# Performance work log

Hardware: AMD Instinct MI355X
Metric: run time of the kernel (lower is better)

The kernel has to match this reference:

```python
import jax, jax.numpy as jnp
import numpy as np

B, D, H, C = 8192, 1024, 4, 4  # batch, input_dim, num_heads, num_classes


def setup_inputs() -> dict:
    key = jax.random.key(0)
    ks = jax.random.split(key, 24)
    s = 0.02
    n = jax.random.normal
    d = {
        "X1": n(ks[0], (B, D), jnp.float32),
        "X2": n(ks[1], (B, D), jnp.float32),
        "X3": n(ks[2], (B, D), jnp.float32),
        "X4": n(ks[3], (B, D), jnp.float32),
        # shared Q projection (injected into both self- and cross-attn at init)
        "Wq": n(ks[4], (D, D), jnp.float32) * s,
        "bq": jnp.zeros((D,), jnp.float32),
        # self-attention K/V/out projections
        "Wk_s": n(ks[5], (D, D), jnp.float32) * s,
        "bk_s": jnp.zeros((D,), jnp.float32),
        "Wv_s": n(ks[6], (D, D), jnp.float32) * s,
        "bv_s": jnp.zeros((D,), jnp.float32),
        "Wo_s": n(ks[7], (D, D), jnp.float32) * s,
        "bo_s": jnp.zeros((D,), jnp.float32),
        # cross-attention K/V/out projections
        "Wk_c": n(ks[8], (D, D), jnp.float32) * s,
        "bk_c": jnp.zeros((D,), jnp.float32),
        "Wv_c": n(ks[9], (D, D), jnp.float32) * s,
        "bv_c": jnp.zeros((D,), jnp.float32),
        "Wo_c": n(ks[10], (D, D), jnp.float32) * s,
        "bo_c": jnp.zeros((D,), jnp.float32),
        # classifier
        "Wc": n(ks[11], (C, D), jnp.float32) * s,
        "bc": jnp.zeros((C,), jnp.float32),
    }
    return d


def _mha(q, kv, Wq, bq, Wk, bk, Wv, bv, Wo, bo):
    # q: (B, Lq, D), kv: (B, Lk, D); matches torch nn.MultiheadAttention math
    Bq, Lq, Dm = q.shape
    Lk = kv.shape[1]
    hd = Dm // H
    Q = (q @ Wq.T + bq).reshape(Bq, Lq, H, hd).transpose(0, 2, 1, 3)
    K = (kv @ Wk.T + bk).reshape(Bq, Lk, H, hd).transpose(0, 2, 1, 3)
    V = (kv @ Wv.T + bv).reshape(Bq, Lk, H, hd).transpose(0, 2, 1, 3)
    scores = jnp.einsum('bhqd,bhkd->bhqk', Q, K) / jnp.sqrt(jnp.float32(hd))
    attn = jax.nn.softmax(scores, axis=-1)
    out = jnp.einsum('bhqk,bhkd->bhqd', attn, V)
    out = out.transpose(0, 2, 1, 3).reshape(Bq, Lq, Dm)
    return out @ Wo.T + bo


def _diff_attn(query, key_list, p):
    # query: (B, D); key_list: list of 3 (B, D)
    q1 = query[:, None, :]  # (B, 1, D)
    self_out = _mha(q1, q1, p['Wq'], p['bq'], p['Wk_s'], p['bk_s'],
                    p['Wv_s'], p['bv_s'], p['Wo_s'], p['bo_s'])
    keys = jnp.stack(key_list, axis=1)          # (B, 3, D)
    differ_keys = q1 - keys                      # (B, 3, D)
    cross_out = _mha(q1, differ_keys, p['Wq'], p['bq'], p['Wk_c'], p['bk_c'],
                     p['Wv_c'], p['bv_c'], p['Wo_c'], p['bo_c'])
    return (self_out + cross_out)[:, 0]          # (B, D)


def reference(X1, X2, X3, X4, Wq, bq, Wk_s, bk_s, Wv_s, bv_s, Wo_s, bo_s,
              Wk_c, bk_c, Wv_c, bv_c, Wo_c, bo_c, Wc, bc):
    p = dict(Wq=Wq, bq=bq, Wk_s=Wk_s, bk_s=bk_s, Wv_s=Wv_s, bv_s=bv_s,
             Wo_s=Wo_s, bo_s=bo_s, Wk_c=Wk_c, bk_c=bk_c, Wv_c=Wv_c,
             bv_c=bv_c, Wo_c=Wo_c, bo_c=bo_c)
    d1 = _diff_attn(X1, [X2, X3, X4], p)
    d2 = _diff_attn(X2, [X1, X3, X4], p)
    d3 = _diff_attn(X3, [X1, X2, X4], p)
    d4 = _diff_attn(X4, [X1, X2, X3], p)
    features = jnp.concatenate([d1, d2, d3, d4], axis=0)  # (4B, D)
    logits = features @ Wc.T + bc                          # (4B, C)
    return (d1, d2, d3, d4, logits)
```

## Files before the change

### kernel.cpp

```cpp
#include <hip/hip_runtime.h>

typedef __bf16 bf16x8 __attribute__((ext_vector_type(8)));
typedef float f32x4 __attribute__((ext_vector_type(4)));

__device__ __forceinline__ float bf2f(unsigned short u) {
  union { unsigned int i; float f; } c; c.i = ((unsigned int)u) << 16; return c.f;
}
__device__ __forceinline__ unsigned short f2bf(float f) {
  union { float f; unsigned int i; } c; c.f = f;
  unsigned int u = c.i;
  u += 0x7FFFu + ((u >> 16) & 1u);
  return (unsigned short)(u >> 16);
}

#define GLDS16(g, l)                                                          \
  __builtin_amdgcn_global_load_lds(                                           \
      (const __attribute__((address_space(1))) void*)(g),                     \
      (__attribute__((address_space(3))) void*)(l), 16, 0, 0)

#define MFMA16(a, b, c) __builtin_amdgcn_mfma_f32_16x16x32_bf16(a, b, c, 0, 0, 0)


__global__ __launch_bounds__(256) void convert_x(
    const float* __restrict__ X1, const float* __restrict__ X2,
    const float* __restrict__ X3, const float* __restrict__ X4,
    unsigned short* __restrict__ Xcat)
{
  int gid = blockIdx.x * 256 + threadIdx.x;
  size_t base = (size_t)gid * 4;
  int sec = (int)(base >> 23);
  int off = (int)(base & 8388607);
  const float* s = sec == 0 ? X1 : sec == 1 ? X2 : sec == 2 ? X3 : X4;
  float4 v = *(const float4*)(s + off);
  ushort4 o;
  o.x = f2bf(v.x); o.y = f2bf(v.y); o.z = f2bf(v.z); o.w = f2bf(v.w);
  *(ushort4*)(Xcat + base) = o;
}

__global__ __launch_bounds__(256) void prep_w(
    const float* __restrict__ Wq,  const float* __restrict__ Wk_c,
    const float* __restrict__ Wv_c, const float* __restrict__ Wo_c,
    const float* __restrict__ Wo_s,
    unsigned short* __restrict__ Wcat, unsigned short* __restrict__ WoM2,
    unsigned short* __restrict__ Wos_bf)
{
  int gid = blockIdx.x * 256 + threadIdx.x;
  if (gid < 786432) {
    int base = gid * 4;
    int sec = base >> 20, off = base & 1048575;
    const float* s = sec == 0 ? Wk_c : sec == 1 ? Wv_c : Wq;
    float4 v = *(const float4*)(s + off);
    ushort4 o;
    o.x = f2bf(v.x); o.y = f2bf(v.y); o.z = f2bf(v.z); o.w = f2bf(v.w);
    *(ushort4*)(Wcat + base) = o;
  } else if (gid < 1048576) {
    int idx = (gid - 786432) * 4;
    int n = idx >> 10, c = idx & 1023;
    float4 v = *(const float4*)(Wo_c + (size_t)n * 1024 + c);
    ushort4 o;
    o.x = f2bf(v.x); o.y = f2bf(v.y); o.z = f2bf(v.z); o.w = f2bf(v.w);
    *(ushort4*)(WoM2 + (size_t)n * 2048 + c) = o;
  } else if (gid < 1310720) {
    int base = (gid - 1048576) * 4;
    float4 v = *(const float4*)(Wo_s + base);
    ushort4 o;
    o.x = f2bf(v.x); o.y = f2bf(v.y); o.z = f2bf(v.z); o.w = f2bf(v.w);
    *(ushort4*)(Wos_bf + base) = o;
  }
}

__global__ __launch_bounds__(256) void transpose_wvs(
    const float* __restrict__ Wv_s, unsigned short* __restrict__ WvsT)
{
  __shared__ float tile[32][33];
  const int r = threadIdx.x >> 3;
  const int c4 = (threadIdx.x & 7) * 4;
  const int j0 = blockIdx.y * 32, k0 = blockIdx.x * 32;
  float4 v = *(const float4*)(Wv_s + (size_t)(j0 + r) * 1024 + k0 + c4);
  tile[r][c4] = v.x; tile[r][c4 + 1] = v.y; tile[r][c4 + 2] = v.z; tile[r][c4 + 3] = v.w;
  __syncthreads();
  ushort4 o;
  o.x = f2bf(tile[c4 + 0][r]); o.y = f2bf(tile[c4 + 1][r]);
  o.z = f2bf(tile[c4 + 2][r]); o.w = f2bf(tile[c4 + 3][r]);
  *(ushort4*)(WvsT + (size_t)(k0 + r) * 1024 + j0 + c4) = o;
}

__global__ __launch_bounds__(256) void bias2_kernel(
    const float* __restrict__ Wo_s, const float* __restrict__ bv_s,
    const float* __restrict__ bo_c, const float* __restrict__ bo_s,
    float* __restrict__ bias2)
{
  const int wv = threadIdx.x >> 6, l = threadIdx.x & 63;
  const int n = blockIdx.x * 4 + wv;
  const float* row = Wo_s + (size_t)n * 1024;
  float s = 0.f;
#pragma unroll
  for (int it = 0; it < 4; ++it) {
    int j = it * 256 + l * 4;
    float4 w = *(const float4*)(row + j);
    float4 b = *(const float4*)(bv_s + j);
    s += w.x * b.x + w.y * b.y + w.z * b.z + w.w * b.w;
  }
#pragma unroll
  for (int d = 1; d < 64; d <<= 1) s += __shfl_xor(s, d);
  if (l == 0) bias2[n] = s + bo_c[n] + bo_s[n];
}

template<bool OUT_F32, bool HAS_BIAS>
__global__ __launch_bounds__(256) void gemm_bt(
    const unsigned short* __restrict__ A1, int lda1, int K1,
    const unsigned short* __restrict__ A2, int lda2, int K2,
    const unsigned short* __restrict__ Bw, int ldb,
    void* __restrict__ Cout, int ldc,
    const float* __restrict__ bias)
{
  __shared__ char lds[16384];
  char* ldsA = lds;
  char* ldsB = lds + 8192;

  const int t = threadIdx.x;
  const int l = t & 63;
  const int wv = t >> 6;
  const int wr = wv >> 1, wc = wv & 1;
  const int bM = blockIdx.y * 128, bN = blockIdx.x * 128;

  const int pa0 = t, pa1 = t + 256;
  const int ra0 = pa0 >> 2, ra1 = pa1 >> 2;
  const int ca0 = (((pa0 & 3) ^ ((ra0 >> 1) & 3))) * 8;
  const int ca1 = (((pa1 & 3) ^ ((ra1 >> 1) & 3))) * 8;
  const unsigned short* gB0 = Bw + (size_t)(bN + ra0) * ldb + ca0;
  const unsigned short* gB1 = Bw + (size_t)(bN + ra1) * ldb + ca1;
  char* lA0 = ldsA + pa0 * 16; char* lA1 = ldsA + pa1 * 16;
  char* lB0 = ldsB + pa0 * 16; char* lB1 = ldsB + pa1 * 16;

  const int rA = wr * 64 + (l & 15);
  const int rB = wc * 64 + (l & 15);
  const int cA = ((l >> 4) ^ ((rA >> 1) & 3)) * 16;
  const int cB = ((l >> 4) ^ ((rB >> 1) & 3)) * 16;
  const char* fA = ldsA + rA * 64 + cA;
  const char* fB = ldsB + rB * 64 + cB;

  f32x4 acc[4][4] = {};

  const unsigned short* gA0 = A1 + (size_t)(bM + ra0) * lda1 + ca0;
  const unsigned short* gA1 = A1 + (size_t)(bM + ra1) * lda1 + ca1;

  for (int src = 0; src < 2; ++src) {
    const int Kc = src ? K2 : K1;
    if (src) {
      if (K2 == 0) break;
      gA0 = A2 + (size_t)(bM + ra0) * lda2 + ca0;
      gA1 = A2 + (size_t)(bM + ra1) * lda2 + ca1;
    }
    for (int k0 = 0; k0 < Kc; k0 += 32) {
      GLDS16(gA0, lA0); GLDS16(gA1, lA1);
      GLDS16(gB0, lB0); GLDS16(gB1, lB1);
      gA0 += 32; gA1 += 32; gB0 += 32; gB1 += 32;
      __syncthreads();

      bf16x8 af[4], bfv[4];
#pragma unroll
      for (int i = 0; i < 4; ++i) af[i] = *(const bf16x8*)(fA + i * 1024);
#pragma unroll
      for (int i = 0; i < 4; ++i) bfv[i] = *(const bf16x8*)(fB + i * 1024);
#pragma unroll
      for (int mt = 0; mt < 4; ++mt)
#pragma unroll
        for (int nt = 0; nt < 4; ++nt)
          acc[mt][nt] = MFMA16(af[mt], bfv[nt], acc[mt][nt]);
      __syncthreads();
    }
  }

  const int mrow = bM + wr * 64 + ((l >> 4) << 2);
  const int ncol = bN + wc * 64 + (l & 15);
  float bvals[4];
  if (HAS_BIAS) {
#pragma unroll
    for (int nt = 0; nt < 4; ++nt) bvals[nt] = bias[ncol + nt * 16];
  }
#pragma unroll
  for (int mt = 0; mt < 4; ++mt)
#pragma unroll
    for (int nt = 0; nt < 4; ++nt)
#pragma unroll
      for (int r = 0; r < 4; ++r) {
        size_t idx = (size_t)(mrow + mt * 16 + r) * ldc + (ncol + nt * 16);
        float v = acc[mt][nt][r];
        if (HAS_BIAS) v += bvals[nt];
        if (OUT_F32) ((float*)Cout)[idx] = v;
        else         ((unsigned short*)Cout)[idx] = f2bf(v);
      }
}

template<bool OUT_F32, bool HAS_BIAS>
__global__ __launch_bounds__(512, 2) void gemm256(
    const unsigned short* __restrict__ A1, int lda1, int K1,
    const unsigned short* __restrict__ A2, int lda2, int K2,
    const unsigned short* __restrict__ Bw, int ldb,
    void* __restrict__ Cout, int ldc,
    const float* __restrict__ bias)
{
  __shared__ __align__(128) char lds[131072];

  const int tid = threadIdx.x;
  const int l  = tid & 63;
  const int wv = tid >> 6;
  const int wr = wv >> 2, wc = wv & 3;

  const int nN = gridDim.x;
  int lin = blockIdx.y * nN + blockIdx.x;
  int nwg = nN * gridDim.y;
  int id2 = ((nwg & 7) == 0) ? ((lin & 7) * (nwg >> 3) + (lin >> 3)) : lin;
  const int bM = (id2 / nN) * 256;
  const int bN = (id2 % nN) * 256;

  const int NT1 = K1 >> 6;
  const int NT  = (K1 + K2) >> 6;

  const int sr0  = tid >> 2;
  const int colE = ((tid & 3) ^ ((sr0 >> 1) & 3)) * 8;
  const unsigned short* pA1g0 = A1 + (size_t)(bM + sr0) * lda1 + colE;
  const unsigned short* pA1g1 = A1 + (size_t)(bM + sr0 + 128) * lda1 + colE;
  const unsigned short* pA2g0 = (K2 > 0) ? A2 + (size_t)(bM + sr0) * lda2 + colE : pA1g0;
  const unsigned short* pA2g1 = (K2 > 0) ? A2 + (size_t)(bM + sr0 + 128) * lda2 + colE : pA1g1;
  const unsigned short* pBg0  = Bw + (size_t)(bN + sr0) * ldb + colE;
  const unsigned short* pBg1  = Bw + (size_t)(bN + sr0 + 128) * ldb + colE;
  char* ldsw = lds + tid * 16;

  auto stageA = [&](int tt, int kh) {
    const unsigned short *p0, *p1; int tc;
    if (tt < NT1) { p0 = pA1g0; p1 = pA1g1; tc = (tt << 6) + (kh << 5); }
    else          { p0 = pA2g0; p1 = pA2g1; tc = ((tt - NT1) << 6) + (kh << 5); }
    unsigned off = (unsigned)((tt & 1) << 16) + (unsigned)(kh << 14);
    GLDS16(p0 + tc, ldsw + off);
    GLDS16(p1 + tc, ldsw + off + 8192);
  };
  auto stageB = [&](int tt, int kh) {
    int tc = (tt << 6) + (kh << 5);
    unsigned off = (unsigned)((tt & 1) << 16) + 32768u + (unsigned)(kh << 14);
    GLDS16(pBg0 + tc, ldsw + off);
    GLDS16(pBg1 + tc, ldsw + off + 8192);
  };

  const int swz = ((l >> 4) ^ (((l & 15) >> 1) & 3)) << 4;
  const char* rdA0 = lds + ((wr * 128 + (l & 15)) * 64 + swz);
  const char* rdB0 = lds + (32768 + (wc * 64 + (l & 15)) * 64 + swz);

  f32x4 acc[8][4] = {};

  stageA(0, 0); stageB(0, 0); stageA(0, 1); stageB(0, 1);
  stageA(1, 0); stageB(1, 0); stageA(1, 1);
  asm volatile("s_waitcnt vmcnt(10)" ::: "memory");
  __builtin_amdgcn_s_barrier();

  for (int t = 0; t < NT; ++t) {
    const char* rA = rdA0 + ((t & 1) << 16);
    const char* rB = rdB0 + ((t & 1) << 16);
    bf16x8 af[8], bfr[4];

    bfr[0] = *(const bf16x8*)(rB);
    bfr[1] = *(const bf16x8*)(rB + 1024);
#pragma unroll
    for (int m = 0; m < 8; ++m) af[m] = *(const bf16x8*)(rA + m * 1024);
    bfr[2] = *(const bf16x8*)(rB + 2048);
    bfr[3] = *(const bf16x8*)(rB + 3072);
    if (t + 1 < NT) stageB(t + 1, 1);
    __builtin_amdgcn_s_setprio(1);
#pragma unroll
    for (int m = 0; m < 8; ++m) {
      acc[m][0] = MFMA16(af[m], bfr[0], acc[m][0]);
      acc[m][1] = MFMA16(af[m], bfr[1], acc[m][1]);
    }
    __builtin_amdgcn_s_setprio(0);
    __builtin_amdgcn_s_barrier();

    if (t + 2 < NT) stageA(t + 2, 0);
    __builtin_amdgcn_s_setprio(1);
#pragma unroll
    for (int m = 0; m < 8; ++m) {
      acc[m][2] = MFMA16(af[m], bfr[2], acc[m][2]);
      acc[m][3] = MFMA16(af[m], bfr[3], acc[m][3]);
    }
    __builtin_amdgcn_s_setprio(0);
    if (t < NT - 2)       asm volatile("s_waitcnt vmcnt(10)" ::: "memory");
    else if (t == NT - 2) asm volatile("s_waitcnt vmcnt(8)" ::: "memory");
    else                  asm volatile("s_waitcnt vmcnt(0)" ::: "memory");
    __builtin_amdgcn_s_barrier();

    bfr[0] = *(const bf16x8*)(rB + 16384);
    bfr[1] = *(const bf16x8*)(rB + 16384 + 1024);
#pragma unroll
    for (int m = 0; m < 8; ++m) af[m] = *(const bf16x8*)(rA + 16384 + m * 1024);
    bfr[2] = *(const bf16x8*)(rB + 16384 + 2048);
    bfr[3] = *(const bf16x8*)(rB + 16384 + 3072);
    if (t + 2 < NT) stageB(t + 2, 0);
    __builtin_amdgcn_s_setprio(1);
#pragma unroll
    for (int m = 0; m < 8; ++m) {
      acc[m][0] = MFMA16(af[m], bfr[0], acc[m][0]);
      acc[m][1] = MFMA16(af[m], bfr[1], acc[m][1]);
    }
    __builtin_amdgcn_s_setprio(0);
    __builtin_amdgcn_s_barrier();

    if (t + 2 < NT) stageA(t + 2, 1);
    __builtin_amdgcn_s_setprio(1);
#pragma unroll
    for (int m = 0; m < 8; ++m) {
      acc[m][2] = MFMA16(af[m], bfr[2], acc[m][2]);
      acc[m][3] = MFMA16(af[m], bfr[3], acc[m][3]);
    }
    __builtin_amdgcn_s_setprio(0);
    if (t < NT - 2)       asm volatile("s_waitcnt vmcnt(10)" ::: "memory");
    else if (t == NT - 2) asm volatile("s_waitcnt vmcnt(4)" ::: "memory");
    else                  asm volatile("s_waitcnt vmcnt(0)" ::: "memory");
    __builtin_amdgcn_s_barrier();
  }

  const int lr0 = wr * 128 + ((l >> 4) << 2);
  const int lc0 = wc * 64 + (l & 15);
  float bvals[4];
  if (HAS_BIAS) {
#pragma unroll
    for (int n = 0; n < 4; ++n) bvals[n] = bias[bN + lc0 + n * 16];
  }

  if (!OUT_F32) {
    unsigned short* lt = (unsigned short*)lds;
    unsigned short* Cp = (unsigned short*)Cout;
#pragma unroll
    for (int m = 0; m < 8; ++m)
#pragma unroll
      for (int n = 0; n < 4; ++n)
#pragma unroll
        for (int r = 0; r < 4; ++r) {
          float v = acc[m][n][r];
          if (HAS_BIAS) v += bvals[n];
          int row = lr0 + m * 16 + r;
          int col = lc0 + n * 16;
          int a = row * 256 + ((((col >> 3) ^ ((row >> 2) & 3)) << 3) | (col & 7));
          lt[a] = f2bf(v);
        }
    __syncthreads();
#pragma unroll
    for (int i = 0; i < 16; ++i) {
      int ch = i * 512 + tid;
      int row = ch >> 5, c = ch & 31;
      uint4 v = *(const uint4*)(lt + row * 256 + ((c ^ ((row >> 2) & 3)) << 3));
      *(uint4*)(Cp + (size_t)(bM + row) * ldc + bN + c * 8) = v;
    }
  } else {
    float* lf = (float*)lds;
    float* Cp = (float*)Cout;
#pragma unroll
    for (int h = 0; h < 2; ++h) {
      if (wr == h) {
        const int lrh = (l >> 4) << 2;
#pragma unroll
        for (int m = 0; m < 8; ++m)
#pragma unroll
          for (int n = 0; n < 4; ++n)
#pragma unroll
            for (int r = 0; r < 4; ++r) {
              float v = acc[m][n][r];
              if (HAS_BIAS) v += bvals[n];
              int row = lrh + m * 16 + r;
              int col = lc0 + n * 16;
              int a = row * 256 + ((((col >> 2) ^ ((row >> 2) & 3)) << 2) | (col & 3));
              lf[a] = v;
            }
      }
      __syncthreads();
#pragma unroll
      for (int i = 0; i < 16; ++i) {
        int ch = i * 512 + tid;
        int row = ch >> 6, c = ch & 63;
        float4 v = *(const float4*)(lf + row * 256 + ((c ^ ((row >> 2) & 3)) << 2));
        *(float4*)(Cp + (size_t)(bM + h * 128 + row) * ldc + bN + c * 4) = v;
      }
      __syncthreads();
    }
  }
}

__global__ __launch_bounds__(256) void attn_kernel(
    unsigned short* __restrict__ Yp,
    const float* __restrict__ bq,  const float* __restrict__ bkc,
    const float* __restrict__ bvc)
{
  const int b = blockIdx.x;
  const int h = threadIdx.x >> 6;
  const int l = threadIdx.x & 63;
  const int e0 = h * 256 + l * 4;

  const float4 bqv = *(const float4*)(bq + e0);
  const float4 bkv = *(const float4*)(bkc + e0);
  const float4 bvv = *(const float4*)(bvc + e0);

  float q[4][4], kc[4][4], vc[4][4];
  size_t rb[4];
#pragma unroll
  for (int i = 0; i < 4; ++i) {
    rb[i] = ((size_t)i * 8192 + b) * 3072;
    ushort4 qq = *(const ushort4*)(Yp + rb[i] + 2048 + e0);
    ushort4 kk = *(const ushort4*)(Yp + rb[i] + e0);
    ushort4 vv = *(const ushort4*)(Yp + rb[i] + 1024 + e0);
    q[i][0] = bf2f(qq.x) + bqv.x; q[i][1] = bf2f(qq.y) + bqv.y;
    q[i][2] = bf2f(qq.z) + bqv.z; q[i][3] = bf2f(qq.w) + bqv.w;
    kc[i][0] = bf2f(kk.x); kc[i][1] = bf2f(kk.y);
    kc[i][2] = bf2f(kk.z); kc[i][3] = bf2f(kk.w);
    vc[i][0] = bf2f(vv.x); vc[i][1] = bf2f(vv.y);
    vc[i][2] = bf2f(vv.z); vc[i][3] = bf2f(vv.w);
  }

  float u[4][4], tb[4];
#pragma unroll
  for (int i = 0; i < 4; ++i) {
    tb[i] = q[i][0]*bkv.x + q[i][1]*bkv.y + q[i][2]*bkv.z + q[i][3]*bkv.w;
#pragma unroll
    for (int j = 0; j < 4; ++j)
      u[i][j] = q[i][0]*kc[j][0] + q[i][1]*kc[j][1] + q[i][2]*kc[j][2] + q[i][3]*kc[j][3];
  }
#pragma unroll
  for (int d = 1; d < 64; d <<= 1) {
#pragma unroll
    for (int i = 0; i < 4; ++i) {
      tb[i] += __shfl_xor(tb[i], d);
#pragma unroll
      for (int j = 0; j < 4; ++j) u[i][j] += __shfl_xor(u[i][j], d);
    }
  }

#pragma unroll
  for (int i = 0; i < 4; ++i) {
    float s[4], a[4];
    float mx = -1e30f;
#pragma unroll
    for (int j = 0; j < 4; ++j) {
      s[j] = (u[i][i] - u[i][j] + tb[i]) * 0.0625f;
      if (j != i) mx = fmaxf(mx, s[j]);
    }
    float den = 0.f;
#pragma unroll
    for (int j = 0; j < 4; ++j) {
      a[j] = (j == i) ? 0.f : __expf(s[j] - mx);
      den += a[j];
    }
    float inv = 1.f / den;
#pragma unroll
    for (int j = 0; j < 4; ++j) a[j] *= inv;

    float o0 = vc[i][0] + bvv.x, o1 = vc[i][1] + bvv.y;
    float o2 = vc[i][2] + bvv.z, o3 = vc[i][3] + bvv.w;
#pragma unroll
    for (int j = 0; j < 4; ++j) {
      o0 -= a[j] * vc[j][0]; o1 -= a[j] * vc[j][1];
      o2 -= a[j] * vc[j][2]; o3 -= a[j] * vc[j][3];
    }
    ushort4 w;
    w.x = f2bf(o0); w.y = f2bf(o1); w.z = f2bf(o2); w.w = f2bf(o3);
    *(ushort4*)(Yp + rb[i] + 2048 + e0) = w;
  }
}

__global__ __launch_bounds__(256) void logits_kernel(
    const float* __restrict__ feats, const float* __restrict__ Wc,
    const float* __restrict__ bc, float* __restrict__ out)
{
  __shared__ float w[4096];
  const int t = threadIdx.x;
  for (int i = t; i < 4096; i += 256) w[i] = Wc[i];
  __syncthreads();
  const int wave = t >> 6, l = t & 63;
  const int row = blockIdx.x * 4 + wave;
  const float* f = feats + (size_t)row * 1024;
  float s0 = 0.f, s1 = 0.f, s2 = 0.f, s3 = 0.f;
#pragma unroll
  for (int c4 = 0; c4 < 4; ++c4) {
    int e = c4 * 256 + l * 4;
    float4 x  = *(const float4*)(f + e);
    float4 w0 = *(const float4*)(w + e);
    float4 w1 = *(const float4*)(w + 1024 + e);
    float4 w2 = *(const float4*)(w + 2048 + e);
    float4 w3 = *(const float4*)(w + 3072 + e);
    s0 += x.x*w0.x + x.y*w0.y + x.z*w0.z + x.w*w0.w;
    s1 += x.x*w1.x + x.y*w1.y + x.z*w1.z + x.w*w1.w;
    s2 += x.x*w2.x + x.y*w2.y + x.z*w2.z + x.w*w2.w;
    s3 += x.x*w3.x + x.y*w3.y + x.z*w3.z + x.w*w3.w;
  }
#pragma unroll
  for (int d = 1; d < 64; d <<= 1) {
    s0 += __shfl_xor(s0, d); s1 += __shfl_xor(s1, d);
    s2 += __shfl_xor(s2, d); s3 += __shfl_xor(s3, d);
  }
  if (l < 4) {
    float s = (l == 0) ? s0 : (l == 1) ? s1 : (l == 2) ? s2 : s3;
    out[(size_t)row * 4 + l] = s + bc[l];
  }
}

extern "C" void kernel_launch(void* const* d_in, const int* in_sizes, int n_in,
                              void* d_out, int out_size, void* d_ws, size_t ws_size,
                              hipStream_t stream) {
  const float* X1   = (const float*)d_in[0];
  const float* X2   = (const float*)d_in[1];
  const float* X3   = (const float*)d_in[2];
  const float* X4   = (const float*)d_in[3];
  const float* Wq   = (const float*)d_in[4];
  const float* bq   = (const float*)d_in[5];
  const float* Wv_s = (const float*)d_in[8];
  const float* bv_s = (const float*)d_in[9];
  const float* Wo_s = (const float*)d_in[10];
  const float* bo_s = (const float*)d_in[11];
  const float* Wk_c = (const float*)d_in[12];
  const float* bk_c = (const float*)d_in[13];
  const float* Wv_c = (const float*)d_in[14];
  const float* bv_c = (const float*)d_in[15];
  const float* Wo_c = (const float*)d_in[16];
  const float* bo_c = (const float*)d_in[17];
  const float* Wc   = (const float*)d_in[18];
  const float* bc   = (const float*)d_in[19];

  char* ws = (char*)d_ws;
  unsigned short* Xcat   = (unsigned short*)(ws + 0);
  unsigned short* Wcat   = (unsigned short*)(ws + 67108864);
  unsigned short* WoM2   = (unsigned short*)(ws + 73400320);
  unsigned short* Wos_bf = (unsigned short*)(ws + 77594624);
  unsigned short* WvsT   = (unsigned short*)(ws + 79691776);
  float*          bias2  = (float*)        (ws + 81788928);
  unsigned short* Yproj  = (unsigned short*)(ws + 81793024);
  float* out = (float*)d_out;

  convert_x<<<32768, 256, 0, stream>>>(X1, X2, X3, X4, Xcat);
  prep_w<<<5120, 256, 0, stream>>>(Wq, Wk_c, Wv_c, Wo_c, Wo_s, Wcat, WoM2, Wos_bf);
  transpose_wvs<<<dim3(32, 32), 256, 0, stream>>>(Wv_s, WvsT);
  bias2_kernel<<<256, 256, 0, stream>>>(Wo_s, bv_s, bo_c, bo_s, bias2);
  gemm_bt<false, false><<<dim3(8, 8), 256, 0, stream>>>(
      Wos_bf, 1024, 1024, nullptr, 0, 0, WvsT, 1024,
      (void*)(WoM2 + 1024), 2048, nullptr);
  gemm256<false, false><<<dim3(12, 128), 512, 0, stream>>>(
      Xcat, 1024, 1024, nullptr, 0, 0, Wcat, 1024,
      (void*)Yproj, 3072, nullptr);
  attn_kernel<<<8192, 256, 0, stream>>>(Yproj, bq, bk_c, bv_c);
  gemm256<true, true><<<dim3(4, 128), 512, 0, stream>>>(
      Yproj + 2048, 3072, 1024, Xcat, 1024, 1024, WoM2, 2048,
      (void*)out, 1024, bias2);
  logits_kernel<<<8192, 256, 0, stream>>>(out, Wc, bc, out + 33554432);
}
```

Baseline: 710.7 us.

## Shorten GEMM prefetch depth, split A-fragment loads, and rework epilogue LDS swizzle

The GEMM main loop now prefetches only one tile ahead instead of two, so the in-flight global→LDS load count drops from 10 to 4. Each half-tile computes 4 M-rows across all 4 N-columns in two phases rather than 8 rows across 2 columns, which halves live A fragments and should lower register pressure. The epilogue LDS swizzle is changed to XOR at 16-element granularity to alter bank-conflict behaviour on the C stores. The shallower prefetch may expose more global-load latency in exchange for fewer registers and waits.

Result: no change. 724.5 us (+1.9%).

```diff
diff --git a/kernel.cpp b/kernel.cpp
--- a/kernel.cpp
+++ b/kernel.cpp
@@ -249,72 +249,78 @@
 
   f32x4 acc[8][4] = {};
 
-  stageA(0, 0); stageB(0, 0); stageA(0, 1); stageB(0, 1);
-  stageA(1, 0); stageB(1, 0); stageA(1, 1);
-  asm volatile("s_waitcnt vmcnt(10)" ::: "memory");
+  stageB(0, 0); stageA(0, 0); stageB(0, 1); stageA(0, 1);
+  asm volatile("s_waitcnt vmcnt(4)" ::: "memory");
   __builtin_amdgcn_s_barrier();
 
   for (int t = 0; t < NT; ++t) {
     const char* rA = rdA0 + ((t & 1) << 16);
     const char* rB = rdB0 + ((t & 1) << 16);
-    bf16x8 af[8], bfr[4];
+    const bool more = (t + 1 < NT);
+    bf16x8 af[4], bfr[4];
 
     bfr[0] = *(const bf16x8*)(rB);
+    af[0]  = *(const bf16x8*)(rA);
     bfr[1] = *(const bf16x8*)(rB + 1024);
-#pragma unroll
-    for (int m = 0; m < 8; ++m) af[m] = *(const bf16x8*)(rA + m * 1024);
+    af[1]  = *(const bf16x8*)(rA + 1024);
     bfr[2] = *(const bf16x8*)(rB + 2048);
+    af[2]  = *(const bf16x8*)(rA + 2048);
     bfr[3] = *(const bf16x8*)(rB + 3072);
-    if (t + 1 < NT) stageB(t + 1, 1);
+    af[3]  = *(const bf16x8*)(rA + 3072);
+    if (more) stageB(t + 1, 0);
     __builtin_amdgcn_s_setprio(1);
 #pragma unroll
-    for (int m = 0; m < 8; ++m) {
-      acc[m][0] = MFMA16(af[m], bfr[0], acc[m][0]);
-      acc[m][1] = MFMA16(af[m], bfr[1], acc[m][1]);
-    }
+    for (int m = 0; m < 4; ++m)
+#pragma unroll
+      for (int n = 0; n < 4; ++n)
+        acc[m][n] = MFMA16(af[m], bfr[n], acc[m][n]);
     __builtin_amdgcn_s_setprio(0);
     __builtin_amdgcn_s_barrier();
 
-    if (t + 2 < NT) stageA(t + 2, 0);
+#pragma unroll
+    for (int m = 0; m < 4; ++m) af[m] = *(const bf16x8*)(rA + (m + 4) * 1024);
+    if (more) stageA(t + 1, 0);
     __builtin_amdgcn_s_setprio(1);
 #pragma unroll
-    for (int m = 0; m < 8; ++m) {
-      acc[m][2] = MFMA16(af[m], bfr[2], acc[m][2]);
-      acc[m][3] = MFMA16(af[m], bfr[3], acc[m][3]);
-    }
+    for (int m = 0; m < 4; ++m)
+#pragma unroll
+      for (int n = 0; n < 4; ++n)
+        acc[m + 4][n] = MFMA16(af[m], bfr[n], acc[m + 4][n]);
     __builtin_amdgcn_s_setprio(0);
-    if (t < NT - 2)       asm volatile("s_waitcnt vmcnt(10)" ::: "memory");
-    else if (t == NT - 2) asm volatile("s_waitcnt vmcnt(8)" ::: "memory");
-    else                  asm volatile("s_waitcnt vmcnt(0)" ::: "memory");
+    if (more) asm volatile("s_waitcnt vmcnt(4)" ::: "memory");
+    else      asm volatile("s_waitcnt vmcnt(0)" ::: "memory");
     __builtin_amdgcn_s_barrier();
 
     bfr[0] = *(const bf16x8*)(rB + 16384);
+    af[0]  = *(const bf16x8*)(rA + 16384);
     bfr[1] = *(const bf16x8*)(rB + 16384 + 1024);
-#pragma unroll
-    for (int m = 0; m < 8; ++m) af[m] = *(const bf16x8*)(rA + 16384 + m * 1024);
+    af[1]  = *(const bf16x8*)(rA + 16384 + 1024);
     bfr[2] = *(const bf16x8*)(rB + 16384 + 2048);
+    af[2]  = *(const bf16x8*)(rA + 16384 + 2048);
     bfr[3] = *(const bf16x8*)(rB + 16384 + 3072);
-    if (t + 2 < NT) stageB(t + 2, 0);
+    af[3]  = *(const bf16x8*)(rA + 16384 + 3072);
+    if (more) stageB(t + 1, 1);
     __builtin_amdgcn_s_setprio(1);
 #pragma unroll
-    for (int m = 0; m < 8; ++m) {
-      acc[m][0] = MFMA16(af[m], bfr[0], acc[m][0]);
-      acc[m][1] = MFMA16(af[m], bfr[1], acc[m][1]);
-    }
+    for (int m = 0; m < 4; ++m)
+#pragma unroll
+      for (int n = 0; n < 4; ++n)
+        acc[m][n] = MFMA16(af[m], bfr[n], acc[m][n]);
     __builtin_amdgcn_s_setprio(0);
     __builtin_amdgcn_s_barrier();
 
-    if (t + 2 < NT) stageA(t + 2, 1);
+#pragma unroll
+    for (int m = 0; m < 4; ++m) af[m] = *(const bf16x8*)(rA + 16384 + (m + 4) * 1024);
+    if (more) stageA(t + 1, 1);
     __builtin_amdgcn_s_setprio(1);
 #pragma unroll
-    for (int m = 0; m < 8; ++m) {
-      acc[m][2] = MFMA16(af[m], bfr[2], acc[m][2]);
-      acc[m][3] = MFMA16(af[m], bfr[3], acc[m][3]);
-    }
+    for (int m = 0; m < 4; ++m)
+#pragma unroll
+      for (int n = 0; n < 4; ++n)
+        acc[m + 4][n] = MFMA16(af[m], bfr[n], acc[m + 4][n]);
     __builtin_amdgcn_s_setprio(0);
-    if (t < NT - 2)       asm volatile("s_waitcnt vmcnt(10)" ::: "memory");
-    else if (t == NT - 2) asm volatile("s_waitcnt vmcnt(4)" ::: "memory");
-    else                  asm volatile("s_waitcnt vmcnt(0)" ::: "memory");
+    if (more) asm volatile("s_waitcnt vmcnt(4)" ::: "memory");
+    else      asm volatile("s_waitcnt vmcnt(0)" ::: "memory");
     __builtin_amdgcn_s_barrier();
   }
 
@@ -339,7 +345,7 @@
           if (HAS_BIAS) v += bvals[n];
           int row = lr0 + m * 16 + r;
           int col = lc0 + n * 16;
-          int a = row * 256 + ((((col >> 3) ^ ((row >> 2) & 3)) << 3) | (col & 7));
+          int a = row * 256 + ((((col >> 4) ^ ((row >> 2) & 3)) << 4) | (col & 15));
           lt[a] = f2bf(v);
         }
     __syncthreads();
@@ -347,7 +353,8 @@
     for (int i = 0; i < 16; ++i) {
       int ch = i * 512 + tid;
       int row = ch >> 5, c = ch & 31;
-      uint4 v = *(const uint4*)(lt + row * 256 + ((c ^ ((row >> 2) & 3)) << 3));
+      int cp = ((c >> 1) ^ ((row >> 2) & 3)) * 2 + (c & 1);
+      uint4 v = *(const uint4*)(lt + row * 256 + cp * 8);
       *(uint4*)(Cp + (size_t)(bM + row) * ldc + bN + c * 8) = v;
     }
   } else {
@@ -367,7 +374,7 @@
               if (HAS_BIAS) v += bvals[n];
               int row = lrh + m * 16 + r;
               int col = lc0 + n * 16;
-              int a = row * 256 + ((((col >> 2) ^ ((row >> 2) & 3)) << 2) | (col & 3));
+              int a = row * 256 + ((((col >> 4) ^ ((row >> 2) & 3)) << 4) | (col & 15));
               lf[a] = v;
             }
       }
@@ -376,7 +383,8 @@
       for (int i = 0; i < 16; ++i) {
         int ch = i * 512 + tid;
         int row = ch >> 6, c = ch & 63;
-        float4 v = *(const float4*)(lf + row * 256 + ((c ^ ((row >> 2) & 3)) << 2));
+        int cq = ((c >> 2) ^ ((row >> 2) & 3)) * 4 + (c & 3);
+        float4 v = *(const float4*)(lf + row * 256 + cq * 4);
         *(float4*)(Cp + (size_t)(bM + h * 128 + row) * ldc + bN + c * 4) = v;
       }
       __syncthreads();
```
